# Optimization experiments

Measured on AMD Instinct MI355X. Metric: run time of the kernel, lower is better.

The kernel has to match this reference:

```python
import jax, jax.numpy as jnp
import numpy as np

VOCAB, D_MODEL, NHEAD, NLAYER, DIM_FF, MAX_LEN = 32000, 1024, 16, 6, 4096, 1024
B, L = 8, 1024
PAD_ID = 0
EPS = 1e-5


def _ln(x, g, b):
    m = x.mean(-1, keepdims=True)
    v = x.var(-1, keepdims=True)
    return (x - m) / jnp.sqrt(v + EPS) * g + b


def _mha(x, Wqkv, bqkv, Wo, bo, kpm):
    # x: [B,L,D]; Wqkv: [3D,D]; kpm: [B,L] bool (True = padded key)
    Bx, Lx, D = x.shape
    dh = D // NHEAD
    qkv = x @ Wqkv.T + bqkv                       # [B,L,3D]
    q, k, v = jnp.split(qkv, 3, axis=-1)
    sp = lambda t: t.reshape(Bx, Lx, NHEAD, dh).transpose(0, 2, 1, 3)  # [B,H,L,dh]
    q, k, v = sp(q), sp(k), sp(v)
    scores = jnp.einsum('bhqd,bhkd->bhqk', q, k) * (dh ** -0.5)
    scores = jnp.where(kpm[:, None, None, :], jnp.asarray(-1e9, scores.dtype), scores)
    attn = jax.nn.softmax(scores, axis=-1)        # explicit weights, as ForceWeightsMHA demands
    o = jnp.einsum('bhqk,bhkd->bhqd', attn, v)
    o = o.transpose(0, 2, 1, 3).reshape(Bx, Lx, D)
    return o @ Wo.T + bo


def setup_inputs() -> dict:
    key = jax.random.key(0)
    ks = jax.random.split(key, 20)
    s = 0.02
    n = lambda k, shp: (jax.random.normal(k, shp, dtype=jnp.float32) * s)
    inp = {
        'input_ids': jax.random.randint(ks[0], (B, L), 0, VOCAB, dtype=jnp.int64) if jax.config.jax_enable_x64 else jax.random.randint(ks[0], (B, L), 0, VOCAB).astype(jnp.int32),
        'tok_emb': n(ks[1], (VOCAB, D_MODEL)),
        'pos_emb': n(ks[2], (MAX_LEN, D_MODEL)),
        'Wqkv': n(ks[3], (NLAYER, 3 * D_MODEL, D_MODEL)),
        'bqkv': jnp.zeros((NLAYER, 3 * D_MODEL), jnp.float32),
        'Wo': n(ks[4], (NLAYER, D_MODEL, D_MODEL)),
        'bo': jnp.zeros((NLAYER, D_MODEL), jnp.float32),
        'ln1_g': jnp.ones((NLAYER, D_MODEL), jnp.float32),
        'ln1_b': jnp.zeros((NLAYER, D_MODEL), jnp.float32),
        'W1': n(ks[5], (NLAYER, DIM_FF, D_MODEL)),
        'b1': jnp.zeros((NLAYER, DIM_FF), jnp.float32),
        'W2': n(ks[6], (NLAYER, D_MODEL, DIM_FF)),
        'b2': jnp.zeros((NLAYER, D_MODEL), jnp.float32),
        'ln2_g': jnp.ones((NLAYER, D_MODEL), jnp.float32),
        'ln2_b': jnp.zeros((NLAYER, D_MODEL), jnp.float32),
        'head_ln_g': jnp.ones((D_MODEL,), jnp.float32),
        'head_ln_b': jnp.zeros((D_MODEL,), jnp.float32),
        'head_W': n(ks[7], (MAX_LEN, D_MODEL)),
        'head_b': jnp.zeros((MAX_LEN,), jnp.float32),
    }
    return inp


def reference(input_ids, tok_emb, pos_emb, Wqkv, bqkv, Wo, bo, ln1_g, ln1_b,
              W1, b1, W2, b2, ln2_g, ln2_b, head_ln_g, head_ln_b, head_W, head_b):
    Bx, Lx = input_ids.shape
    x = tok_emb[input_ids] + pos_emb[None, :Lx]           # [B,L,D]
    kpm = (input_ids == PAD_ID).at[:, 0].set(False)        # key padding mask, col 0 forced valid
    for i in range(NLAYER):                                # post-norm encoder layer (PyTorch default)
        x = _ln(x + _mha(x, Wqkv[i], bqkv[i], Wo[i], bo[i], kpm), ln1_g[i], ln1_b[i])
        ff = jax.nn.gelu(x @ W1[i].T + b1[i], approximate=False) @ W2[i].T + b2[i]
        x = _ln(x + ff, ln2_g[i], ln2_b[i])
    cls = x[:, 0, :]                                       # [B,D]
    return _ln(cls, head_ln_g, head_ln_b) @ head_W.T + head_b  # [B,MAX_LEN]
```

## Files before the change

### kernel.cpp

```cpp
#include <hip/hip_runtime.h>
#include <cstdint>

#define D_MODEL 1024
#define NHEAD   16
#define NLAYER  6
#define DIM_FF  4096
#define SEQ_B   8
#define SEQ_L   1024
#define TOKENS  (SEQ_B*SEQ_L)

typedef __bf16 v8bf  __attribute__((ext_vector_type(8)));
typedef __bf16 v4bf  __attribute__((ext_vector_type(4)));
typedef float  v4f   __attribute__((ext_vector_type(4)));

__device__ __forceinline__ void gl_lds16(const void* g, void* l) {
  __builtin_amdgcn_global_load_lds(
      (const __attribute__((address_space(1))) void*)g,
      (__attribute__((address_space(3))) void*)l, 16, 0, 0);
}

__device__ __forceinline__ float gelu_f(float x) {
  float z = fabsf(x) * 0.70710678118f;
  float t = __builtin_amdgcn_rcpf(1.f + 0.3275911f * z);
  float p = t * (0.254829592f + t * (-0.284496736f +
            t * (1.421413741f + t * (-1.453152027f + t * 1.061405429f))));
  float e = __expf(-z * z);
  float erfz = 1.f - p * e;
  return 0.5f * x * (1.f + copysignf(erfz, x));
}

__global__ __launch_bounds__(256) void f2b_kernel(const float4* __restrict__ in,
                                                  ushort4* __restrict__ out, long n4) {
  long i = (long)blockIdx.x * 256 + threadIdx.x;
  long stride = (long)gridDim.x * 256;
  for (; i < n4; i += stride) {
    float4 v = in[i];
    v4bf r = { (__bf16)v.x, (__bf16)v.y, (__bf16)v.z, (__bf16)v.w };
    out[i] = *(ushort4*)&r;
  }
}

__global__ __launch_bounds__(256) void embed_kernel(const int* __restrict__ ids,
    const float4* __restrict__ tok, const float4* __restrict__ pos,
    float4* __restrict__ X, ushort4* __restrict__ Xb) {
  long i = (long)blockIdx.x * 256 + threadIdx.x;
  int d4 = (int)(i & 255);
  long bl = i >> 8;
  int l = (int)(bl & (SEQ_L - 1));
  int id = ids[bl];
  float4 t = tok[(long)id * 256 + d4];
  float4 p = pos[(long)l * 256 + d4];
  float4 v = {t.x + p.x, t.y + p.y, t.z + p.z, t.w + p.w};
  X[i] = v;
  v4bf r = { (__bf16)v.x, (__bf16)v.y, (__bf16)v.z, (__bf16)v.w };
  Xb[i] = *(ushort4*)&r;
}

__global__ __launch_bounds__(256) void maskb_kernel(const int* __restrict__ ids,
                                                    float* __restrict__ mb) {
  int i = blockIdx.x * 256 + threadIdx.x;
  mb[i] = (ids[i] == 0 && (i & 1023) != 0) ? -1e9f : 0.f;
}

#define MM16(AF, BF, FO) \
  { _Pragma("unroll") for (int f_ = 0; f_ < 4; ++f_) { \
      _Pragma("unroll") for (int j_ = 0; j_ < 4; ++j_) \
        acc[(FO)+f_][j_] = __builtin_amdgcn_mfma_f32_16x16x32_bf16(AF[f_], BF[j_], acc[(FO)+f_][j_], 0, 0, 0); } }
#define MM8(AF, BF, FO) \
  { _Pragma("unroll") for (int f_ = 0; f_ < 4; ++f_) { \
      _Pragma("unroll") for (int j_ = 0; j_ < 2; ++j_) \
        acc[(FO)+f_][j_] = __builtin_amdgcn_mfma_f32_16x16x32_bf16(AF[f_], BF[j_], acc[(FO)+f_][j_], 0, 0, 0); } }

#define STA(c,h,kt) { const unsigned short* s_ = pA + (long)(m0 + (h)*128)*K + ((long)(kt)<<6); \
  gl_lds16(s_,                 dAs + (c)*16384 + (h)*8192); \
  gl_lds16(s_ + ((long)K<<6),  dAs + (c)*16384 + (h)*8192 + 4096); }
#define STB(c,h,kt) { const unsigned short* s_ = pW + (long)(n0 + (h)*128)*K + ((long)(kt)<<6); \
  gl_lds16(s_,                 dBs + (c)*16384 + (h)*8192); \
  gl_lds16(s_ + ((long)K<<6),  dBs + (c)*16384 + (h)*8192 + 4096); }
#define STB2(c,kt) { const unsigned short* s_ = pW + (long)n0*K + ((long)(kt)<<6); \
  gl_lds16(s_,                 dBs + (c)*8192); \
  gl_lds16(s_ + ((long)K<<6),  dBs + (c)*8192 + 4096); }

#define LGKM0  asm volatile("s_waitcnt lgkmcnt(0)" ::: "memory")
#define VMCNT6 asm volatile("s_waitcnt vmcnt(6)" ::: "memory")
#define VMCNT8 asm volatile("s_waitcnt vmcnt(8)" ::: "memory")
#define BARR   __builtin_amdgcn_s_barrier()
#define SCHED0 __builtin_amdgcn_sched_barrier(0)

#define GTILE(asP, bsP, c, ktn) { \
    v8bf aA[4], aB[4], aC[4], aD[4], bA[4], bB[4]; \
    _Pragma("unroll") for (int f = 0; f < 4; ++f) aA[f] = *(const v8bf*)(asP + offA[f]); \
    _Pragma("unroll") for (int j = 0; j < 4; ++j) bA[j] = *(const v8bf*)(bsP + offB[j]); \
    _Pragma("unroll") for (int j = 0; j < 4; ++j) bB[j] = *(const v8bf*)(bsP + (offB[j] ^ 32)); \
    __builtin_amdgcn_s_setprio(1); MM16(aA, bA, 0); __builtin_amdgcn_s_setprio(0); \
    _Pragma("unroll") for (int f = 0; f < 4; ++f) aB[f] = *(const v8bf*)(asP + (offA[f] ^ 32)); \
    _Pragma("unroll") for (int f = 0; f < 4; ++f) aC[f] = *(const v8bf*)(asP + offA[4 + f]); \
    _Pragma("unroll") for (int f = 0; f < 4; ++f) aD[f] = *(const v8bf*)(asP + (offA[4 + f] ^ 32)); \
    __builtin_amdgcn_s_setprio(1); MM16(aB, bB, 0); __builtin_amdgcn_s_setprio(0); \
    LGKM0; BARR; SCHED0; \
    STA(c, 0, ktn); STB(c, 0, ktn); \
    __builtin_amdgcn_s_setprio(1); MM16(aC, bA, 4); __builtin_amdgcn_s_setprio(0); \
    STA(c, 1, ktn); STB(c, 1, ktn); \
    __builtin_amdgcn_s_setprio(1); MM16(aD, bB, 4); __builtin_amdgcn_s_setprio(0); \
    VMCNT8; BARR; SCHED0; \
  }

#define NTILE(asP, bsP, c, ktn) { \
    v8bf aA[4], aB[4], aC[4], aD[4], bA[2], bB[2]; \
    _Pragma("unroll") for (int f = 0; f < 4; ++f) aA[f] = *(const v8bf*)(asP + offA[f]); \
    _Pragma("unroll") for (int j = 0; j < 2; ++j) bA[j] = *(const v8bf*)(bsP + offB[j]); \
    _Pragma("unroll") for (int j = 0; j < 2; ++j) bB[j] = *(const v8bf*)(bsP + (offB[j] ^ 32)); \
    __builtin_amdgcn_s_setprio(1); MM8(aA, bA, 0); __builtin_amdgcn_s_setprio(0); \
    _Pragma("unroll") for (int f = 0; f < 4; ++f) aB[f] = *(const v8bf*)(asP + (offA[f] ^ 32)); \
    _Pragma("unroll") for (int f = 0; f < 4; ++f) aC[f] = *(const v8bf*)(asP + offA[4 + f]); \
    _Pragma("unroll") for (int f = 0; f < 4; ++f) aD[f] = *(const v8bf*)(asP + (offA[4 + f] ^ 32)); \
    __builtin_amdgcn_s_setprio(1); MM8(aB, bB, 0); __builtin_amdgcn_s_setprio(0); \
    LGKM0; BARR; SCHED0; \
    STA(c, 0, ktn); STB2(c, ktn); \
    __builtin_amdgcn_s_setprio(1); MM8(aC, bA, 4); __builtin_amdgcn_s_setprio(0); \
    STA(c, 1, ktn); \
    __builtin_amdgcn_s_setprio(1); MM8(aD, bB, 4); __builtin_amdgcn_s_setprio(0); \
    VMCNT6; BARR; SCHED0; \
  }

template<int EPI>
__global__ __launch_bounds__(512, 2) void gemm256(
    const unsigned short* __restrict__ A,
    const unsigned short* __restrict__ W,
    const float* __restrict__ bias,
    unsigned short* __restrict__ Cb,
    unsigned short* __restrict__ Vt,
    int M, int N, int K) {
  __shared__ unsigned short As[2][16384];
  __shared__ unsigned short Bs[2][16384];
  int tid = threadIdx.x;
  int wave = tid >> 6, lane = tid & 63;
  int l15 = lane & 15, quad = lane >> 4;
  int wm = wave >> 2;
  int wn = wave & 3;

  int id = blockIdx.y * gridDim.x + blockIdx.x;
  int xcd = id & 7, sidx = id >> 3;
  int mt = xcd * 4 + (sidx & 3);
  int nt = sidx >> 2;
  int m0 = mt * 256, n0 = nt * 256;

  int srow = tid >> 3;
  int scol = ((tid & 7) ^ ((tid >> 4) & 7)) << 3;
  const unsigned short* pA = A + (long)srow * K + scol;
  const unsigned short* pW = W + (long)srow * K + scol;
  unsigned short* dAs = &As[0][0] + (tid << 3);
  unsigned short* dBs = &Bs[0][0] + (tid << 3);

  int offA[8], offB[4];
  #pragma unroll
  for (int f = 0; f < 8; ++f) {
    int r = wm * 128 + f * 16 + l15;
    offA[f] = r * 64 + ((quad ^ ((r >> 1) & 7)) << 3);
  }
  #pragma unroll
  for (int j = 0; j < 4; ++j) {
    int r = wn * 64 + j * 16 + l15;
    offB[j] = r * 64 + ((quad ^ ((r >> 1) & 7)) << 3);
  }

  v4f acc[8][4];
  #pragma unroll
  for (int f = 0; f < 8; ++f)
    #pragma unroll
    for (int j = 0; j < 4; ++j) acc[f][j] = (v4f){0.f, 0.f, 0.f, 0.f};

  int KT = K >> 6;
  STA(0, 0, 0); STB(0, 0, 0); STA(0, 1, 0); STB(0, 1, 0);
  STA(1, 0, 1); STB(1, 0, 1); STA(1, 1, 1); STB(1, 1, 1);
  VMCNT8; BARR; SCHED0;

  const unsigned short* as0 = &As[0][0];
  const unsigned short* bs0 = &Bs[0][0];
  const unsigned short* as1 = &As[1][0];
  const unsigned short* bs1 = &Bs[1][0];

  for (int tb = 0; tb < KT; tb += 2) {
    int kt2 = (tb + 2 < KT) ? tb + 2 : KT - 1;
    int kt3 = (tb + 3 < KT) ? tb + 3 : KT - 1;
    GTILE(as0, bs0, 0, kt2);
    GTILE(as1, bs1, 1, kt3);
  }

  #pragma unroll
  for (int f = 0; f < 8; ++f) {
    int crow0 = m0 + wm * 128 + f * 16 + quad * 4;
    #pragma unroll
    for (int j = 0; j < 4; ++j) {
      int col = n0 + wn * 64 + j * 16 + l15;
      float bv = bias[col];
      if (EPI == 3 && col >= 2048) {
        int hc = (col - 2048) >> 6, d = (col - 2048) & 63;
        int bb = crow0 >> 10, l = crow0 & 1023;
        v4bf pk = { (__bf16)(acc[f][j][0] + bv), (__bf16)(acc[f][j][1] + bv),
                    (__bf16)(acc[f][j][2] + bv), (__bf16)(acc[f][j][3] + bv) };
        *(ushort4*)&Vt[((long)((bb * 16 + hc) * 64 + d)) * 1024 + l] = *(ushort4*)&pk;
      } else {
        #pragma unroll
        for (int r = 0; r < 4; ++r) {
          float v = acc[f][j][r] + bv;
          if (EPI == 1) v = gelu_f(v);
          ((__bf16*)Cb)[(long)(crow0 + r) * N + col] = (__bf16)v;
        }
      }
    }
  }
}

__global__ __launch_bounds__(512, 2) void gemm256n(
    const unsigned short* __restrict__ A,
    const unsigned short* __restrict__ W,
    const float* __restrict__ bias,
    float* __restrict__ Cf,
    int M, int N, int K) {
  __shared__ unsigned short As[2][16384];
  __shared__ unsigned short Bs[2][8192];
  int tid = threadIdx.x;
  int wave = tid >> 6, lane = tid & 63;
  int l15 = lane & 15, quad = lane >> 4;
  int wm = wave >> 2;
  int wn = wave & 3;

  int id = blockIdx.y * gridDim.x + blockIdx.x;
  int xcd = id & 7, sidx = id >> 3;
  int mt = xcd * 4 + (sidx & 3);
  int nt = sidx >> 2;
  int m0 = mt * 256, n0 = nt * 128;

  int srow = tid >> 3;
  int scol = ((tid & 7) ^ ((tid >> 4) & 7)) << 3;
  const unsigned short* pA = A + (long)srow * K + scol;
  const unsigned short* pW = W + (long)srow * K + scol;
  unsigned short* dAs = &As[0][0] + (tid << 3);
  unsigned short* dBs = &Bs[0][0] + (tid << 3);

  int offA[8], offB[2];
  #pragma unroll
  for (int f = 0; f < 8; ++f) {
    int r = wm * 128 + f * 16 + l15;
    offA[f] = r * 64 + ((quad ^ ((r >> 1) & 7)) << 3);
  }
  #pragma unroll
  for (int j = 0; j < 2; ++j) {
    int r = wn * 32 + j * 16 + l15;
    offB[j] = r * 64 + ((quad ^ ((r >> 1) & 7)) << 3);
  }

  v4f acc[8][2];
  #pragma unroll
  for (int f = 0; f < 8; ++f)
    #pragma unroll
    for (int j = 0; j < 2; ++j) acc[f][j] = (v4f){0.f, 0.f, 0.f, 0.f};

  int KT = K >> 6;
  STA(0, 0, 0); STB2(0, 0); STA(0, 1, 0);
  STA(1, 0, 1); STB2(1, 1); STA(1, 1, 1);
  VMCNT6; BARR; SCHED0;

  const unsigned short* as0 = &As[0][0];
  const unsigned short* bs0 = &Bs[0][0];
  const unsigned short* as1 = &As[1][0];
  const unsigned short* bs1 = &Bs[1][0];

  for (int tb = 0; tb < KT; tb += 2) {
    int kt2 = (tb + 2 < KT) ? tb + 2 : KT - 1;
    int kt3 = (tb + 3 < KT) ? tb + 3 : KT - 1;
    NTILE(as0, bs0, 0, kt2);
    NTILE(as1, bs1, 1, kt3);
  }

  #pragma unroll
  for (int f = 0; f < 8; ++f) {
    int crow0 = m0 + wm * 128 + f * 16 + quad * 4;
    #pragma unroll
    for (int j = 0; j < 2; ++j) {
      int col = n0 + wn * 32 + j * 16 + l15;
      float bv = bias[col];
      #pragma unroll
      for (int r = 0; r < 4; ++r)
        Cf[(long)(crow0 + r) * N + col] = acc[f][j][r] + bv;
    }
  }
}

#define PSP 72
__global__ __launch_bounds__(256) void attn2(
    const unsigned short* __restrict__ QKVb,
    const unsigned short* __restrict__ Vtg,
    const float* __restrict__ mb,
    unsigned short* __restrict__ Ob) {
  __shared__ unsigned short Ks[64 * 64];
  __shared__ unsigned short Vs[64 * 64];
  __shared__ unsigned short Ps[4][16 * PSP];
  int tid = threadIdx.x, wave = tid >> 6, lane = tid & 63;
  int l15 = lane & 15, quad = lane >> 4;
  int b = blockIdx.z, h = blockIdx.y, q0 = blockIdx.x * 64;

  int qrow = q0 + wave * 16 + l15;
  const unsigned short* qb = QKVb + (long)(b * 1024 + qrow) * 3072 + h * 64;
  v8bf gq0 = *(const v8bf*)(qb + quad * 8);
  v8bf gq1 = *(const v8bf*)(qb + 32 + quad * 8);

  v8bf bones;
  #pragma unroll
  for (int j = 0; j < 8; ++j) bones[j] = (l15 == 0) ? (__bf16)1.0f : (__bf16)0.0f;

  float m_run[4], l_run[4];
  v4f O[4];
  #pragma unroll
  for (int r = 0; r < 4; ++r) { m_run[r] = -1e30f; l_run[r] = 0.f; }
  #pragma unroll
  for (int j = 0; j < 4; ++j) O[j] = (v4f){0.f, 0.f, 0.f, 0.f};

  const unsigned short* kgb = QKVb + (long)b * 1024 * 3072 + 1024 + h * 64;
  const unsigned short* vgb = Vtg + (long)((b * 16 + h) * 64) * 1024;
  const float* mrow = mb + b * 1024;

  int srow = tid >> 3;
  int ssl  = (tid & 7) ^ (srow & 7);
  int ph0 = (quad ^ (l15 & 7)) << 3;
  int ph1 = ((quad + 4) ^ (l15 & 7)) << 3;
  const float SC = 0.18033688011112042f;

  for (int k0 = 0; k0 < SEQ_L; k0 += 64) {
    __syncthreads();
    gl_lds16(kgb + (long)(k0 + srow) * 3072 + ssl * 8, &Ks[tid * 8]);
    gl_lds16(kgb + (long)(k0 + srow + 32) * 3072 + ssl * 8, &Ks[tid * 8 + 2048]);
    gl_lds16(vgb + (long)srow * 1024 + k0 + ssl * 8, &Vs[tid * 8]);
    gl_lds16(vgb + (long)(srow + 32) * 1024 + k0 + ssl * 8, &Vs[tid * 8 + 2048]);
    __syncthreads();

    float p[4][4], mr[4];
    #pragma unroll
    for (int r = 0; r < 4; ++r) mr[r] = -1e30f;
    #pragma unroll
    for (int t = 0; t < 4; ++t) {
      int kr = t * 16 + l15;
      v8bf kf0 = *(const v8bf*)&Ks[kr * 64 + ph0];
      v8bf kf1 = *(const v8bf*)&Ks[kr * 64 + ph1];
      v4f s = (v4f){0.f, 0.f, 0.f, 0.f};
      s = __builtin_amdgcn_mfma_f32_16x16x32_bf16(gq0, kf0, s, 0, 0, 0);
      s = __builtin_amdgcn_mfma_f32_16x16x32_bf16(gq1, kf1, s, 0, 0, 0);
      float bv = mrow[k0 + kr];
      #pragma unroll
      for (int r = 0; r < 4; ++r) {
        float sv = fmaf(s[r], SC, bv);
        p[t][r] = sv;
        mr[r] = fmaxf(mr[r], sv);
      }
    }
    #pragma unroll
    for (int r = 0; r < 4; ++r) {
      mr[r] = fmaxf(mr[r], __shfl_xor(mr[r], 1, 64));
      mr[r] = fmaxf(mr[r], __shfl_xor(mr[r], 2, 64));
      mr[r] = fmaxf(mr[r], __shfl_xor(mr[r], 4, 64));
      mr[r] = fmaxf(mr[r], __shfl_xor(mr[r], 8, 64));
    }
    float alpha[4];
    #pragma unroll
    for (int r = 0; r < 4; ++r) {
      float mn = fmaxf(m_run[r], mr[r]);
      alpha[r] = __builtin_amdgcn_exp2f(m_run[r] - mn);
      m_run[r] = mn;
    }
    #pragma unroll
    for (int t = 0; t < 4; ++t)
      #pragma unroll
      for (int r = 0; r < 4; ++r)
        p[t][r] = __builtin_amdgcn_exp2f(p[t][r] - m_run[r]);

    #pragma unroll
    for (int t = 0; t < 4; ++t)
      #pragma unroll
      for (int r = 0; r < 4; ++r)
        ((__bf16*)Ps[wave])[(quad * 4 + r) * PSP + t * 16 + l15] = (__bf16)p[t][r];
    v8bf pa0 = *(const v8bf*)&Ps[wave][l15 * PSP + quad * 8];
    v8bf pa1 = *(const v8bf*)&Ps[wave][l15 * PSP + 32 + quad * 8];

    v4f ss = (v4f){0.f, 0.f, 0.f, 0.f};
    ss = __builtin_amdgcn_mfma_f32_16x16x32_bf16(pa0, bones, ss, 0, 0, 0);
    ss = __builtin_amdgcn_mfma_f32_16x16x32_bf16(pa1, bones, ss, 0, 0, 0);

    #pragma unroll
    for (int j = 0; j < 4; ++j)
      #pragma unroll
      for (int r = 0; r < 4; ++r) O[j][r] *= alpha[r];
    #pragma unroll
    for (int j = 0; j < 4; ++j) {
      v8bf vf0 = *(const v8bf*)&Vs[(j * 16 + l15) * 64 + ph0];
      v8bf vf1 = *(const v8bf*)&Vs[(j * 16 + l15) * 64 + ph1];
      O[j] = __builtin_amdgcn_mfma_f32_16x16x32_bf16(pa0, vf0, O[j], 0, 0, 0);
      O[j] = __builtin_amdgcn_mfma_f32_16x16x32_bf16(pa1, vf1, O[j], 0, 0, 0);
    }
    #pragma unroll
    for (int r = 0; r < 4; ++r)
      l_run[r] = l_run[r] * alpha[r] + __shfl(ss[r], quad << 4, 64);
  }

  int qd = q0 + wave * 16 + quad * 4;
  #pragma unroll
  for (int r = 0; r < 4; ++r) {
    float inv = 1.f / l_run[r];
    #pragma unroll
    for (int j = 0; j < 4; ++j)
      ((__bf16*)Ob)[(long)(b * 1024 + qd + r) * 1024 + h * 64 + j * 16 + l15] =
          (__bf16)(O[j][r] * inv);
  }
}

__global__ __launch_bounds__(256) void add_ln(
    const float* __restrict__ Xin, const float* __restrict__ Yin,
    const float* __restrict__ g, const float* __restrict__ bta,
    float* __restrict__ outF, unsigned short* __restrict__ outB,
    long in_stride, long out_stride) {
  int row = blockIdx.x;
  const float* x = Xin + (long)row * in_stride;
  const float* y = Yin ? Yin + (long)row * 1024 : nullptr;
  int tid = threadIdx.x;
  float v[4];
  float s = 0.f, s2 = 0.f;
  #pragma unroll
  for (int j = 0; j < 4; ++j) {
    int d = j * 256 + tid;
    float t = x[d] + (y ? y[d] : 0.f);
    v[j] = t; s += t; s2 += t * t;
  }
  __shared__ float red[8];
  int lane = tid & 63, wave = tid >> 6;
  #pragma unroll
  for (int o = 32; o > 0; o >>= 1) { s += __shfl_down(s, o, 64); s2 += __shfl_down(s2, o, 64); }
  if (lane == 0) { red[wave] = s; red[4 + wave] = s2; }
  __syncthreads();
  s  = red[0] + red[1] + red[2] + red[3];
  s2 = red[4] + red[5] + red[6] + red[7];
  float mean = s * (1.f / 1024.f);
  float var  = s2 * (1.f / 1024.f) - mean * mean;
  float rstd = rsqrtf(var + 1e-5f);
  float* of = outF + (long)row * out_stride;
  unsigned short* ob = outB ? outB + (long)row * out_stride : nullptr;
  #pragma unroll
  for (int j = 0; j < 4; ++j) {
    int d = j * 256 + tid;
    float o = (v[j] - mean) * rstd * g[d] + bta[d];
    of[d] = o;
    if (ob) ((__bf16*)ob)[d] = (__bf16)o;
  }
}

__global__ __launch_bounds__(256) void head_kernel(
    const float* __restrict__ cls, const float* __restrict__ hW,
    const float* __restrict__ hb, float* __restrict__ out) {
  int n = blockIdx.x * 256 + threadIdx.x;
  int b = blockIdx.y;
  const float4* c4 = (const float4*)(cls + b * 1024);
  const float4* w4 = (const float4*)(hW + (long)n * 1024);
  float s = 0.f;
  #pragma unroll 8
  for (int d = 0; d < 256; ++d) {
    float4 a = c4[d], w = w4[d];
    s += a.x * w.x + a.y * w.y + a.z * w.z + a.w * w.w;
  }
  out[b * 1024 + n] = s + hb[n];
}

extern "C" void kernel_launch(void* const* d_in, const int* in_sizes, int n_in,
                              void* d_out, int out_size, void* d_ws, size_t ws_size,
                              hipStream_t stream) {
  const int*   ids  = (const int*)d_in[0];
  const float* tok  = (const float*)d_in[1];
  const float* pos  = (const float*)d_in[2];
  const float* Wqkv = (const float*)d_in[3];
  const float* bqkv = (const float*)d_in[4];
  const float* Wo   = (const float*)d_in[5];
  const float* bo   = (const float*)d_in[6];
  const float* ln1g = (const float*)d_in[7];
  const float* ln1b = (const float*)d_in[8];
  const float* W1   = (const float*)d_in[9];
  const float* b1   = (const float*)d_in[10];
  const float* W2   = (const float*)d_in[11];
  const float* b2   = (const float*)d_in[12];
  const float* ln2g = (const float*)d_in[13];
  const float* ln2b = (const float*)d_in[14];
  const float* hlng = (const float*)d_in[15];
  const float* hlnb = (const float*)d_in[16];
  const float* hW   = (const float*)d_in[17];
  const float* hb   = (const float*)d_in[18];
  float* out = (float*)d_out;

  char* ws = (char*)d_ws;
  size_t off = 0;
  auto alloc = [&](size_t bytes) {
    char* p = ws + off;
    off = (off + bytes + 255) & ~(size_t)255;
    return p;
  };
  unsigned short* Wqkv_b = (unsigned short*)alloc((size_t)NLAYER*3072*1024*2);
  unsigned short* Wo_b   = (unsigned short*)alloc((size_t)NLAYER*1024*1024*2);
  unsigned short* W1_b   = (unsigned short*)alloc((size_t)NLAYER*4096*1024*2);
  unsigned short* W2_b   = (unsigned short*)alloc((size_t)NLAYER*1024*4096*2);
  float*          X      = (float*)alloc((size_t)TOKENS*1024*4);
  unsigned short* Xb     = (unsigned short*)alloc((size_t)TOKENS*1024*2);
  unsigned short* Qb     = (unsigned short*)alloc((size_t)TOKENS*3072*2);
  unsigned short* Vtg    = (unsigned short*)alloc((size_t)TOKENS*1024*2);
  float*          Y      = (float*)alloc((size_t)TOKENS*1024*4);
  unsigned short* Ab     = (unsigned short*)alloc((size_t)TOKENS*1024*2);
  unsigned short* Gb     = Qb;
  float*          cls    = (float*)alloc(8*1024*4);
  float*          mb     = (float*)alloc(TOKENS*4);

  f2b_kernel<<<2048, 256, 0, stream>>>((const float4*)Wqkv, (ushort4*)Wqkv_b, (long)NLAYER*3072*1024/4);
  f2b_kernel<<<2048, 256, 0, stream>>>((const float4*)Wo,   (ushort4*)Wo_b,   (long)NLAYER*1024*1024/4);
  f2b_kernel<<<2048, 256, 0, stream>>>((const float4*)W1,   (ushort4*)W1_b,   (long)NLAYER*4096*1024/4);
  f2b_kernel<<<2048, 256, 0, stream>>>((const float4*)W2,   (ushort4*)W2_b,   (long)NLAYER*1024*4096/4);
  embed_kernel<<<(TOKENS*256)/256, 256, 0, stream>>>(ids, (const float4*)tok, (const float4*)pos,
                                                     (float4*)X, (ushort4*)Xb);
  maskb_kernel<<<TOKENS/256, 256, 0, stream>>>(ids, mb);

  for (int i = 0; i < NLAYER; ++i) {
    gemm256<3><<<dim3(3072/256, TOKENS/256), 512, 0, stream>>>(
        Xb, Wqkv_b + (size_t)i*3072*1024, bqkv + i*3072, Qb, Vtg, TOKENS, 3072, 1024);
    attn2<<<dim3(SEQ_L/64, NHEAD, SEQ_B), 256, 0, stream>>>(Qb, Vtg, mb, Ab);
    gemm256n<<<dim3(1024/128, TOKENS/256), 512, 0, stream>>>(
        Ab, Wo_b + (size_t)i*1024*1024, bo + i*1024, Y, TOKENS, 1024, 1024);
    add_ln<<<TOKENS, 256, 0, stream>>>(X, Y, ln1g + i*1024, ln1b + i*1024, X, Xb, 1024L, 1024L);
    gemm256<1><<<dim3(4096/256, TOKENS/256), 512, 0, stream>>>(
        Xb, W1_b + (size_t)i*4096*1024, b1 + i*4096, Gb, nullptr, TOKENS, 4096, 1024);
    gemm256n<<<dim3(1024/128, TOKENS/256), 512, 0, stream>>>(
        Gb, W2_b + (size_t)i*1024*4096, b2 + i*1024, Y, TOKENS, 1024, 4096);
    add_ln<<<TOKENS, 256, 0, stream>>>(X, Y, ln2g + i*1024, ln2b + i*1024, X, Xb, 1024L, 1024L);
  }
  add_ln<<<8, 256, 0, stream>>>(X, nullptr, hlng, hlnb, cls, nullptr, (long)SEQ_L*1024, 1024L);
  head_kernel<<<dim3(4, 8), 256, 0, stream>>>(cls, hW, hb, out);
}
```

Before: 2.781 ms.

## Double-buffer K/V tiles in attention kernel with async prefetch

The attention kernel now keeps two LDS buffers for K and V and prefetches the next 64-key tile with global_load_lds while the current tile is being processed. A vmcnt wait plus barrier replaces the two syncthreads per iteration. MFMA sections are also wrapped in s_setprio to favour matrix issue. This doubles the K/V LDS footprint, which may lower occupancy, and the last iteration issues a redundant reload of the final tile.

```diff
diff --git a/kernel.cpp b/kernel.cpp
--- a/kernel.cpp
+++ b/kernel.cpp
@@ -82,6 +82,7 @@
   gl_lds16(s_ + ((long)K<<6),  dBs + (c)*8192 + 4096); }
 
 #define LGKM0  asm volatile("s_waitcnt lgkmcnt(0)" ::: "memory")
+#define VMCNT4 asm volatile("s_waitcnt vmcnt(4)" ::: "memory")
 #define VMCNT6 asm volatile("s_waitcnt vmcnt(6)" ::: "memory")
 #define VMCNT8 asm volatile("s_waitcnt vmcnt(8)" ::: "memory")
 #define BARR   __builtin_amdgcn_s_barrier()
@@ -289,13 +290,19 @@
 }
 
 #define PSP 72
+#define ASTAGE(c, kt) { int kk = (kt) << 6; \
+    gl_lds16(kgb + (long)(kk + srow) * 3072 + ssl * 8, &Ks[c][tid * 8]); \
+    gl_lds16(kgb + (long)(kk + srow + 32) * 3072 + ssl * 8, &Ks[c][tid * 8 + 2048]); \
+    gl_lds16(vgb + (long)srow * 1024 + kk + ssl * 8, &Vs[c][tid * 8]); \
+    gl_lds16(vgb + (long)(srow + 32) * 1024 + kk + ssl * 8, &Vs[c][tid * 8 + 2048]); }
+
 __global__ __launch_bounds__(256) void attn2(
     const unsigned short* __restrict__ QKVb,
     const unsigned short* __restrict__ Vtg,
     const float* __restrict__ mb,
     unsigned short* __restrict__ Ob) {
-  __shared__ unsigned short Ks[64 * 64];
-  __shared__ unsigned short Vs[64 * 64];
+  __shared__ unsigned short Ks[2][64 * 64];
+  __shared__ unsigned short Vs[2][64 * 64];
   __shared__ unsigned short Ps[4][16 * PSP];
   int tid = threadIdx.x, wave = tid >> 6, lane = tid & 63;
   int l15 = lane & 15, quad = lane >> 4;
@@ -327,30 +334,34 @@
   int ph1 = ((quad + 4) ^ (l15 & 7)) << 3;
   const float SC = 0.18033688011112042f;
 
-  for (int k0 = 0; k0 < SEQ_L; k0 += 64) {
-    __syncthreads();
-    gl_lds16(kgb + (long)(k0 + srow) * 3072 + ssl * 8, &Ks[tid * 8]);
-    gl_lds16(kgb + (long)(k0 + srow + 32) * 3072 + ssl * 8, &Ks[tid * 8 + 2048]);
-    gl_lds16(vgb + (long)srow * 1024 + k0 + ssl * 8, &Vs[tid * 8]);
-    gl_lds16(vgb + (long)(srow + 32) * 1024 + k0 + ssl * 8, &Vs[tid * 8 + 2048]);
-    __syncthreads();
+  ASTAGE(0, 0);
+
+  for (int t = 0; t < SEQ_L / 64; ++t) {
+    int tn = (t + 1 < SEQ_L / 64) ? t + 1 : SEQ_L / 64 - 1;
+    ASTAGE((t + 1) & 1, tn);
+    VMCNT4; BARR; SCHED0;
+    const unsigned short* KsP = Ks[t & 1];
+    const unsigned short* VsP = Vs[t & 1];
+    int k0 = t << 6;
 
     float p[4][4], mr[4];
     #pragma unroll
     for (int r = 0; r < 4; ++r) mr[r] = -1e30f;
     #pragma unroll
-    for (int t = 0; t < 4; ++t) {
-      int kr = t * 16 + l15;
-      v8bf kf0 = *(const v8bf*)&Ks[kr * 64 + ph0];
-      v8bf kf1 = *(const v8bf*)&Ks[kr * 64 + ph1];
+    for (int tt = 0; tt < 4; ++tt) {
+      int kr = tt * 16 + l15;
+      v8bf kf0 = *(const v8bf*)&KsP[kr * 64 + ph0];
+      v8bf kf1 = *(const v8bf*)&KsP[kr * 64 + ph1];
       v4f s = (v4f){0.f, 0.f, 0.f, 0.f};
+      __builtin_amdgcn_s_setprio(1);
       s = __builtin_amdgcn_mfma_f32_16x16x32_bf16(gq0, kf0, s, 0, 0, 0);
       s = __builtin_amdgcn_mfma_f32_16x16x32_bf16(gq1, kf1, s, 0, 0, 0);
+      __builtin_amdgcn_s_setprio(0);
       float bv = mrow[k0 + kr];
       #pragma unroll
       for (int r = 0; r < 4; ++r) {
         float sv = fmaf(s[r], SC, bv);
-        p[t][r] = sv;
+        p[tt][r] = sv;
         mr[r] = fmaxf(mr[r], sv);
       }
     }
@@ -369,16 +380,16 @@
       m_run[r] = mn;
     }
     #pragma unroll
-    for (int t = 0; t < 4; ++t)
+    for (int tt = 0; tt < 4; ++tt)
       #pragma unroll
       for (int r = 0; r < 4; ++r)
-        p[t][r] = __builtin_amdgcn_exp2f(p[t][r] - m_run[r]);
-
-    #pragma unroll
-    for (int t = 0; t < 4; ++t)
+        p[tt][r] = __builtin_amdgcn_exp2f(p[tt][r] - m_run[r]);
+
+    #pragma unroll
+    for (int tt = 0; tt < 4; ++tt)
       #pragma unroll
       for (int r = 0; r < 4; ++r)
-        ((__bf16*)Ps[wave])[(quad * 4 + r) * PSP + t * 16 + l15] = (__bf16)p[t][r];
+        ((__bf16*)Ps[wave])[(quad * 4 + r) * PSP + tt * 16 + l15] = (__bf16)p[tt][r];
     v8bf pa0 = *(const v8bf*)&Ps[wave][l15 * PSP + quad * 8];
     v8bf pa1 = *(const v8bf*)&Ps[wave][l15 * PSP + 32 + quad * 8];
 
@@ -390,16 +401,19 @@
     for (int j = 0; j < 4; ++j)
       #pragma unroll
       for (int r = 0; r < 4; ++r) O[j][r] *= alpha[r];
+    __builtin_amdgcn_s_setprio(1);
     #pragma unroll
     for (int j = 0; j < 4; ++j) {
-      v8bf vf0 = *(const v8bf*)&Vs[(j * 16 + l15) * 64 + ph0];
-      v8bf vf1 = *(const v8bf*)&Vs[(j * 16 + l15) * 64 + ph1];
+      v8bf vf0 = *(const v8bf*)&VsP[(j * 16 + l15) * 64 + ph0];
+      v8bf vf1 = *(const v8bf*)&VsP[(j * 16 + l15) * 64 + ph1];
       O[j] = __builtin_amdgcn_mfma_f32_16x16x32_bf16(pa0, vf0, O[j], 0, 0, 0);
       O[j] = __builtin_amdgcn_mfma_f32_16x16x32_bf16(pa1, vf1, O[j], 0, 0, 0);
     }
+    __builtin_amdgcn_s_setprio(0);
     #pragma unroll
     for (int r = 0; r < 4; ++r)
       l_run[r] = l_run[r] * alpha[r] + __shfl(ss[r], quad << 4, 64);
+    BARR;
   }
 
   int qd = q0 + wave * 16 + quad * 4;
```

Measured after the change: 2.887 ms. +3.8%, slower.
